# Kernel optimization log

Measured on AMD Instinct MI355X. Metric: run time of the kernel, lower is better.

## Reference

```python
import jax, jax.numpy as jnp
import numpy as np

N, D = 16384, 64      # samples, state dimension (input_size)
H1, H2 = 256, 256     # hidden widths


def setup_inputs() -> dict:
    key = jax.random.key(0)
    ks = jax.random.split(key, 7)
    S = jax.random.normal(ks[0], (N, D), jnp.float32)
    Sdot = jax.random.normal(ks[1], (N, D), jnp.float32)
    W1 = jax.random.normal(ks[2], (H1, D), jnp.float32) / np.float32(np.sqrt(D))
    b1 = jax.random.normal(ks[3], (H1,), jnp.float32) * 0.1
    W2 = jax.random.normal(ks[4], (H2, H1), jnp.float32) / np.float32(np.sqrt(H1))
    b2 = jax.random.normal(ks[5], (H2,), jnp.float32) * 0.1
    W3 = jax.random.normal(ks[6], (1, H2), jnp.float32) / np.float32(np.sqrt(H2))
    return {"S": S, "Sdot": Sdot, "W1": W1, "b1": b1, "W2": W2, "b2": b2, "W3": W3}


def _forward_tensors(S, layers, W_last):
    # Manual MLP forward with per-sample Jacobian propagation.
    # SQUARE activation: act(z) = z^2, act'(z) = 2z.
    # torch's diag_embed(act_der) @ J is fused as elementwise row-scaling.
    n, d = S.shape
    y = S
    J = jnp.broadcast_to(jnp.eye(d, dtype=S.dtype), (n, d, d))  # [N, d, d]
    for W, b in layers:
        z = y @ W.T + b                      # [N, h]
        J = jnp.einsum('hp,npd->nhd', W, J)  # W @ J per sample
        J = (2.0 * z)[:, :, None] * J        # diag(2z) @ J as row scaling
        y = z * z                            # SQUARE activation
    nn_out = (y @ W_last.T)[:, 0]            # [N]
    grad_nn = jnp.einsum('h,nhd->nd', W_last[0], J)  # [N, d]
    return nn_out, grad_nn


def reference(S, Sdot, W1, b1, W2, b2, W3):
    nn_out, grad_nn = _forward_tensors(S, [(W1, b1), (W2, b2)], W3)
    circle = jnp.sum(S * S, axis=1)          # [N]
    F = circle
    dF = 2.0 * S
    V = nn_out * F
    gradV = nn_out[:, None] * dF + grad_nn * F[:, None]  # product rule
    Vdot = jnp.sum(gradV * Sdot, axis=1)
    return (V, Vdot, circle)
```

## Files before the change

### kernel.cpp

```cpp
#include <hip/hip_runtime.h>

typedef __attribute__((ext_vector_type(8))) short bf16x8;
typedef __attribute__((ext_vector_type(4))) float f32x4;

constexpr int N  = 16384;
constexpr int D  = 64;
constexpr int H  = 256;
constexpr int SB = 32;
constexpr int PITCH = 272;
constexpr int PLANE = 32 * PITCH;
constexpr int STAGE = 8 * PITCH;

__device__ __forceinline__ ushort f2bf(float x) {
    uint u = __float_as_uint(x);
    u += 0x7fffu + ((u >> 16) & 1u);
    return (ushort)(u >> 16);
}
__device__ __forceinline__ float bf2f(ushort h) {
    return __uint_as_float(((uint)h) << 16);
}
__device__ __forceinline__ int swz(int g, int i) {
    return i ^ ((i >> 2) & 3) ^ ((g & 1) << 1);
}

__global__ void prep_weights(const float* __restrict__ W1, const float* __restrict__ W2,
                             ushort* __restrict__ ws) {
    const int t = blockIdx.x * 256 + threadIdx.x;
    if (t < 8192) {
        const int h1g = t >> 8;
        const int h2  = t & 255;
        const float* src = W2 + h2 * 256 + h1g * 8;
        bf16x8 hi;
        #pragma unroll
        for (int j = 0; j < 8; ++j) hi[j] = (short)f2bf(src[j]);
        *reinterpret_cast<bf16x8*>(ws + 32768 + (h1g * 256 + h2) * 8) = hi;
    } else if (t < 10240) {
        const int u  = t - 8192;
        const int dg = u >> 8;
        const int h1 = u & 255;
        const float* src = W1 + h1 * 64 + dg * 8;
        bf16x8 hi, lo;
        #pragma unroll
        for (int j = 0; j < 8; ++j) {
            const float x = src[j];
            const ushort xh = f2bf(x);
            hi[j] = (short)xh;
            lo[j] = (short)f2bf(x - bf2f(xh));
        }
        const int d1 = (dg * 256 + h1) * 8;
        *reinterpret_cast<bf16x8*>(ws + d1)         = hi;
        *reinterpret_cast<bf16x8*>(ws + 16384 + d1) = lo;
    }
}

__global__ __launch_bounds__(256, 2) void fused_mfma(
    const float* __restrict__ S,  const float* __restrict__ Sdot,
    const float* __restrict__ b1v, const float* __restrict__ b2v,
    const float* __restrict__ W3, const ushort* __restrict__ ws,
    float* __restrict__ out)
{
    __shared__ ushort U[4 * STAGE + 2 * PLANE];
    __shared__ float  red[2][4][32];
    __shared__ float  csd[32][2];

    ushort* const sH = U;
    ushort* const sL = U + STAGE;
    ushort* const dH = U + 2 * STAGE;
    ushort* const dL = U + 3 * STAGE;
    ushort* const yH = U + 4 * STAGE;
    ushort* const pH = U + 4 * STAGE + PLANE;

    const int t   = threadIdx.x;
    const int l   = t & 63;
    const int wid = t >> 6;
    const int lg  = l >> 4;
    const int lc  = l & 15;
    const int s0  = blockIdx.x * SB;

    int hh[4];
    #pragma unroll
    for (int tt = 0; tt < 4; ++tt) hh[tt] = (wid * 4 + tt) * 16 + lc;

    bf16x8 B1h[2][4], B1l[2][4];
    #pragma unroll
    for (int kc = 0; kc < 2; ++kc) {
        const int g = kc * 4 + lg;
        #pragma unroll
        for (int tt = 0; tt < 4; ++tt) {
            const int o = (g * 256 + hh[tt]) * 8;
            B1h[kc][tt] = *reinterpret_cast<const bf16x8*>(ws + o);
            B1l[kc][tt] = *reinterpret_cast<const bf16x8*>(ws + 16384 + o);
        }
    }
    bf16x8 nbh[4];
    #pragma unroll
    for (int tt = 0; tt < 4; ++tt)
        nbh[tt] = *reinterpret_cast<const bf16x8*>(ws + 32768 + (lg * 256 + hh[tt]) * 8);

    float bb1[4], bb2[4], w3v[4];
    #pragma unroll
    for (int tt = 0; tt < 4; ++tt) {
        bb1[tt] = b1v[hh[tt]]; bb2[tt] = b2v[hh[tt]]; w3v[tt] = W3[hh[tt]];
    }

    {
        const int i = t >> 3;
        const int g = t & 7;
        const float* sp = S    + (size_t)(s0 + i) * D + g * 8;
        const float* dp = Sdot + (size_t)(s0 + i) * D + g * 8;
        const float4 s_a = reinterpret_cast<const float4*>(sp)[0];
        const float4 s_b = reinterpret_cast<const float4*>(sp)[1];
        const float4 d_a = reinterpret_cast<const float4*>(dp)[0];
        const float4 d_b = reinterpret_cast<const float4*>(dp)[1];
        const float sv[8] = {s_a.x,s_a.y,s_a.z,s_a.w,s_b.x,s_b.y,s_b.z,s_b.w};
        const float dv[8] = {d_a.x,d_a.y,d_a.z,d_a.w,d_b.x,d_b.y,d_b.z,d_b.w};
        bf16x8 vsh, vsl, vdh, vdl;
        float c = 0.f, sd = 0.f;
        #pragma unroll
        for (int j = 0; j < 8; ++j) {
            c  += sv[j] * sv[j];
            sd += sv[j] * dv[j];
            const ushort hs = f2bf(sv[j]);
            vsh[j] = (short)hs; vsl[j] = (short)f2bf(sv[j] - bf2f(hs));
            const ushort hd = f2bf(dv[j]);
            vdh[j] = (short)hd; vdl[j] = (short)f2bf(dv[j] - bf2f(hd));
        }
        const int off = g * PITCH + swz(g, i) * 8;
        *reinterpret_cast<bf16x8*>(&sH[off]) = vsh;
        *reinterpret_cast<bf16x8*>(&sL[off]) = vsl;
        *reinterpret_cast<bf16x8*>(&dH[off]) = vdh;
        *reinterpret_cast<bf16x8*>(&dL[off]) = vdl;
        #pragma unroll
        for (int o = 1; o < 8; o <<= 1) { c += __shfl_xor(c, o); sd += __shfl_xor(sd, o); }
        if (g == 0) { csd[i][0] = c; csd[i][1] = sd; }
    }
    __syncthreads();

    f32x4 z1acc[2][4], u1acc[2][4];
    #pragma unroll
    for (int mt = 0; mt < 2; ++mt)
        #pragma unroll
        for (int tt = 0; tt < 4; ++tt) {
            z1acc[mt][tt] = (f32x4){0,0,0,0};
            u1acc[mt][tt] = (f32x4){0,0,0,0};
        }
    #pragma unroll
    for (int kc = 0; kc < 2; ++kc) {
        const int g = kc * 4 + lg;
        bf16x8 ash[2], asl[2], adh[2], adl[2];
        #pragma unroll
        for (int mt = 0; mt < 2; ++mt) {
            const int off = g * PITCH + swz(g, mt * 16 + lc) * 8;
            ash[mt] = *reinterpret_cast<const bf16x8*>(&sH[off]);
            asl[mt] = *reinterpret_cast<const bf16x8*>(&sL[off]);
            adh[mt] = *reinterpret_cast<const bf16x8*>(&dH[off]);
            adl[mt] = *reinterpret_cast<const bf16x8*>(&dL[off]);
        }
        __builtin_amdgcn_s_setprio(1);
        #pragma unroll
        for (int tt = 0; tt < 4; ++tt) {
            #pragma unroll
            for (int mt = 0; mt < 2; ++mt) {
                z1acc[mt][tt] = __builtin_amdgcn_mfma_f32_16x16x32_bf16(ash[mt], B1h[kc][tt], z1acc[mt][tt], 0,0,0);
                z1acc[mt][tt] = __builtin_amdgcn_mfma_f32_16x16x32_bf16(asl[mt], B1h[kc][tt], z1acc[mt][tt], 0,0,0);
                z1acc[mt][tt] = __builtin_amdgcn_mfma_f32_16x16x32_bf16(ash[mt], B1l[kc][tt], z1acc[mt][tt], 0,0,0);
                u1acc[mt][tt] = __builtin_amdgcn_mfma_f32_16x16x32_bf16(adh[mt], B1h[kc][tt], u1acc[mt][tt], 0,0,0);
                u1acc[mt][tt] = __builtin_amdgcn_mfma_f32_16x16x32_bf16(adl[mt], B1h[kc][tt], u1acc[mt][tt], 0,0,0);
                u1acc[mt][tt] = __builtin_amdgcn_mfma_f32_16x16x32_bf16(adh[mt], B1l[kc][tt], u1acc[mt][tt], 0,0,0);
            }
        }
        __builtin_amdgcn_s_setprio(0);
    }

    #pragma unroll
    for (int tt = 0; tt < 4; ++tt) {
        const int grp = hh[tt] >> 3;
        const int jb  = grp * PITCH + (hh[tt] & 7);
        #pragma unroll
        for (int mt = 0; mt < 2; ++mt) {
            #pragma unroll
            for (int r = 0; r < 4; ++r) {
                const float z  = z1acc[mt][tt][r] + bb1[tt];
                const float pv = 2.f * z * u1acc[mt][tt][r];
                const int ii = swz(grp, mt * 16 + lg * 4 + r);
                yH[jb + ii * 8] = f2bf(z * z);
                pH[jb + ii * 8] = f2bf(pv);
            }
        }
    }
    __syncthreads();

    f32x4 z2acc[2][4], qacc[2][4];
    #pragma unroll
    for (int mt = 0; mt < 2; ++mt)
        #pragma unroll
        for (int tt = 0; tt < 4; ++tt) {
            z2acc[mt][tt] = (f32x4){0,0,0,0};
            qacc[mt][tt]  = (f32x4){0,0,0,0};
        }
    #pragma unroll 2
    for (int kc = 0; kc < 8; ++kc) {
        const int g = kc * 4 + lg;
        bf16x8 bh[4];
        #pragma unroll
        for (int tt = 0; tt < 4; ++tt) bh[tt] = nbh[tt];
        if (kc < 7) {
            const int gn = (kc + 1) * 4 + lg;
            #pragma unroll
            for (int tt = 0; tt < 4; ++tt)
                nbh[tt] = *reinterpret_cast<const bf16x8*>(ws + 32768 + (gn * 256 + hh[tt]) * 8);
        }
        bf16x8 ayh[2], aph[2];
        #pragma unroll
        for (int mt = 0; mt < 2; ++mt) {
            const int off = g * PITCH + swz(g, mt * 16 + lc) * 8;
            ayh[mt] = *reinterpret_cast<const bf16x8*>(&yH[off]);
            aph[mt] = *reinterpret_cast<const bf16x8*>(&pH[off]);
        }
        __builtin_amdgcn_s_setprio(1);
        #pragma unroll
        for (int tt = 0; tt < 4; ++tt) {
            #pragma unroll
            for (int mt = 0; mt < 2; ++mt) {
                z2acc[mt][tt] = __builtin_amdgcn_mfma_f32_16x16x32_bf16(ayh[mt], bh[tt], z2acc[mt][tt], 0,0,0);
                qacc[mt][tt]  = __builtin_amdgcn_mfma_f32_16x16x32_bf16(aph[mt], bh[tt], qacc[mt][tt], 0,0,0);
            }
        }
        __builtin_amdgcn_s_setprio(0);
    }

    float nnp[2][4], gdp[2][4];
    #pragma unroll
    for (int mt = 0; mt < 2; ++mt)
        #pragma unroll
        for (int r = 0; r < 4; ++r) { nnp[mt][r] = 0.f; gdp[mt][r] = 0.f; }
    #pragma unroll
    for (int tt = 0; tt < 4; ++tt) {
        #pragma unroll
        for (int mt = 0; mt < 2; ++mt) {
            #pragma unroll
            for (int r = 0; r < 4; ++r) {
                const float z = z2acc[mt][tt][r] + bb2[tt];
                nnp[mt][r] += w3v[tt] * z * z;
                gdp[mt][r] += 2.f * w3v[tt] * z * qacc[mt][tt][r];
            }
        }
    }
    #pragma unroll
    for (int mt = 0; mt < 2; ++mt)
        #pragma unroll
        for (int r = 0; r < 4; ++r) {
            float a = nnp[mt][r], b = gdp[mt][r];
            #pragma unroll
            for (int o = 1; o < 16; o <<= 1) { a += __shfl_xor(a, o); b += __shfl_xor(b, o); }
            if (lc == 0) {
                red[0][wid][mt * 16 + lg * 4 + r] = a;
                red[1][wid][mt * 16 + lg * 4 + r] = b;
            }
        }
    __syncthreads();

    if (t < SB) {
        const int i = t;
        float nn = 0.f, gd = 0.f;
        #pragma unroll
        for (int w = 0; w < 4; ++w) { nn += red[0][w][i]; gd += red[1][w][i]; }
        const float c  = csd[i][0];
        const float sd = csd[i][1];
        const int n = s0 + i;
        out[n]         = nn * c;
        out[N + n]     = 2.f * nn * sd + c * gd;
        out[2 * N + n] = c;
    }
}

extern "C" void kernel_launch(void* const* d_in, const int* in_sizes, int n_in,
                              void* d_out, int out_size, void* d_ws, size_t ws_size,
                              hipStream_t stream) {
    const float* S    = (const float*)d_in[0];
    const float* Sdot = (const float*)d_in[1];
    const float* W1   = (const float*)d_in[2];
    const float* b1   = (const float*)d_in[3];
    const float* W2   = (const float*)d_in[4];
    const float* b2   = (const float*)d_in[5];
    const float* W3   = (const float*)d_in[6];
    float* out = (float*)d_out;
    ushort* ws = (ushort*)d_ws;

    prep_weights<<<40, 256, 0, stream>>>(W1, W2, ws);
    fused_mfma<<<N / SB, 256, 0, stream>>>(S, Sdot, b1, b2, W3, ws, out);
}
```

Before: 20.94 us.

## Split hidden dimension across eight waves per block instead of four

```diff
diff --git a/kernel.cpp b/kernel.cpp
--- a/kernel.cpp
+++ b/kernel.cpp
@@ -1,6 +1,7 @@
 #include <hip/hip_runtime.h>
 
 typedef __attribute__((ext_vector_type(8))) short bf16x8;
+typedef __attribute__((ext_vector_type(4))) short bf16x4;
 typedef __attribute__((ext_vector_type(4))) float f32x4;
 
 constexpr int N  = 16384;
@@ -53,14 +54,14 @@
     }
 }
 
-__global__ __launch_bounds__(256, 2) void fused_mfma(
+__global__ __launch_bounds__(512, 4) void fused_mfma(
     const float* __restrict__ S,  const float* __restrict__ Sdot,
     const float* __restrict__ b1v, const float* __restrict__ b2v,
     const float* __restrict__ W3, const ushort* __restrict__ ws,
     float* __restrict__ out)
 {
     __shared__ ushort U[4 * STAGE + 2 * PLANE];
-    __shared__ float  red[2][4][32];
+    __shared__ float  red[2][8][32];
     __shared__ float  csd[32][2];
 
     ushort* const sH = U;
@@ -77,47 +78,27 @@
     const int lc  = l & 15;
     const int s0  = blockIdx.x * SB;
 
-    int hh[4];
-    #pragma unroll
-    for (int tt = 0; tt < 4; ++tt) hh[tt] = (wid * 4 + tt) * 16 + lc;
-
-    bf16x8 B1h[2][4], B1l[2][4];
-    #pragma unroll
-    for (int kc = 0; kc < 2; ++kc) {
-        const int g = kc * 4 + lg;
-        #pragma unroll
-        for (int tt = 0; tt < 4; ++tt) {
-            const int o = (g * 256 + hh[tt]) * 8;
-            B1h[kc][tt] = *reinterpret_cast<const bf16x8*>(ws + o);
-            B1l[kc][tt] = *reinterpret_cast<const bf16x8*>(ws + 16384 + o);
-        }
-    }
-    bf16x8 nbh[4];
-    #pragma unroll
-    for (int tt = 0; tt < 4; ++tt)
-        nbh[tt] = *reinterpret_cast<const bf16x8*>(ws + 32768 + (lg * 256 + hh[tt]) * 8);
-
-    float bb1[4], bb2[4], w3v[4];
-    #pragma unroll
-    for (int tt = 0; tt < 4; ++tt) {
-        bb1[tt] = b1v[hh[tt]]; bb2[tt] = b2v[hh[tt]]; w3v[tt] = W3[hh[tt]];
-    }
+    const int hA = (wid * 2 + 0) * 16 + lc;
+    const int hB = (wid * 2 + 1) * 16 + lc;
+
+    const float bb1[2] = { b1v[hA], b1v[hB] };
+    const float bb2[2] = { b2v[hA], b2v[hB] };
+    const float w3v[2] = { W3[hA],  W3[hB]  };
 
     {
-        const int i = t >> 3;
-        const int g = t & 7;
-        const float* sp = S    + (size_t)(s0 + i) * D + g * 8;
-        const float* dp = Sdot + (size_t)(s0 + i) * D + g * 8;
-        const float4 s_a = reinterpret_cast<const float4*>(sp)[0];
-        const float4 s_b = reinterpret_cast<const float4*>(sp)[1];
-        const float4 d_a = reinterpret_cast<const float4*>(dp)[0];
-        const float4 d_b = reinterpret_cast<const float4*>(dp)[1];
-        const float sv[8] = {s_a.x,s_a.y,s_a.z,s_a.w,s_b.x,s_b.y,s_b.z,s_b.w};
-        const float dv[8] = {d_a.x,d_a.y,d_a.z,d_a.w,d_b.x,d_b.y,d_b.z,d_b.w};
-        bf16x8 vsh, vsl, vdh, vdl;
+        const int i    = t >> 4;
+        const int sub  = t & 15;
+        const int g    = sub >> 1;
+        const int half = sub & 1;
+        const size_t rb = (size_t)(s0 + i) * D + g * 8 + half * 4;
+        const float4 s4 = *reinterpret_cast<const float4*>(S    + rb);
+        const float4 d4 = *reinterpret_cast<const float4*>(Sdot + rb);
+        const float sv[4] = {s4.x, s4.y, s4.z, s4.w};
+        const float dv[4] = {d4.x, d4.y, d4.z, d4.w};
+        bf16x4 vsh, vsl, vdh, vdl;
         float c = 0.f, sd = 0.f;
         #pragma unroll
-        for (int j = 0; j < 8; ++j) {
+        for (int j = 0; j < 4; ++j) {
             c  += sv[j] * sv[j];
             sd += sv[j] * dv[j];
             const ushort hs = f2bf(sv[j]);
@@ -125,28 +106,37 @@
             const ushort hd = f2bf(dv[j]);
             vdh[j] = (short)hd; vdl[j] = (short)f2bf(dv[j] - bf2f(hd));
         }
-        const int off = g * PITCH + swz(g, i) * 8;
-        *reinterpret_cast<bf16x8*>(&sH[off]) = vsh;
-        *reinterpret_cast<bf16x8*>(&sL[off]) = vsl;
-        *reinterpret_cast<bf16x8*>(&dH[off]) = vdh;
-        *reinterpret_cast<bf16x8*>(&dL[off]) = vdl;
-        #pragma unroll
-        for (int o = 1; o < 8; o <<= 1) { c += __shfl_xor(c, o); sd += __shfl_xor(sd, o); }
-        if (g == 0) { csd[i][0] = c; csd[i][1] = sd; }
+        const int off = g * PITCH + swz(g, i) * 8 + half * 4;
+        *reinterpret_cast<bf16x4*>(&sH[off]) = vsh;
+        *reinterpret_cast<bf16x4*>(&sL[off]) = vsl;
+        *reinterpret_cast<bf16x4*>(&dH[off]) = vdh;
+        *reinterpret_cast<bf16x4*>(&dL[off]) = vdl;
+        #pragma unroll
+        for (int o = 1; o < 16; o <<= 1) { c += __shfl_xor(c, o); sd += __shfl_xor(sd, o); }
+        if (sub == 0) { csd[i][0] = c; csd[i][1] = sd; }
     }
     __syncthreads();
 
-    f32x4 z1acc[2][4], u1acc[2][4];
-    #pragma unroll
-    for (int mt = 0; mt < 2; ++mt)
-        #pragma unroll
-        for (int tt = 0; tt < 4; ++tt) {
+    f32x4 z1acc[2][2], u1acc[2][2];
+    #pragma unroll
+    for (int mt = 0; mt < 2; ++mt)
+        #pragma unroll
+        for (int tt = 0; tt < 2; ++tt) {
             z1acc[mt][tt] = (f32x4){0,0,0,0};
             u1acc[mt][tt] = (f32x4){0,0,0,0};
         }
     #pragma unroll
     for (int kc = 0; kc < 2; ++kc) {
         const int g = kc * 4 + lg;
+        bf16x8 bh[2], bl[2];
+        {
+            const int oA = (g * 256 + hA) * 8;
+            const int oB = (g * 256 + hB) * 8;
+            bh[0] = *reinterpret_cast<const bf16x8*>(ws + oA);
+            bh[1] = *reinterpret_cast<const bf16x8*>(ws + oB);
+            bl[0] = *reinterpret_cast<const bf16x8*>(ws + 16384 + oA);
+            bl[1] = *reinterpret_cast<const bf16x8*>(ws + 16384 + oB);
+        }
         bf16x8 ash[2], asl[2], adh[2], adl[2];
         #pragma unroll
         for (int mt = 0; mt < 2; ++mt) {
@@ -158,24 +148,29 @@
         }
         __builtin_amdgcn_s_setprio(1);
         #pragma unroll
-        for (int tt = 0; tt < 4; ++tt) {
+        for (int tt = 0; tt < 2; ++tt) {
             #pragma unroll
             for (int mt = 0; mt < 2; ++mt) {
-                z1acc[mt][tt] = __builtin_amdgcn_mfma_f32_16x16x32_bf16(ash[mt], B1h[kc][tt], z1acc[mt][tt], 0,0,0);
-                z1acc[mt][tt] = __builtin_amdgcn_mfma_f32_16x16x32_bf16(asl[mt], B1h[kc][tt], z1acc[mt][tt], 0,0,0);
-                z1acc[mt][tt] = __builtin_amdgcn_mfma_f32_16x16x32_bf16(ash[mt], B1l[kc][tt], z1acc[mt][tt], 0,0,0);
-                u1acc[mt][tt] = __builtin_amdgcn_mfma_f32_16x16x32_bf16(adh[mt], B1h[kc][tt], u1acc[mt][tt], 0,0,0);
-                u1acc[mt][tt] = __builtin_amdgcn_mfma_f32_16x16x32_bf16(adl[mt], B1h[kc][tt], u1acc[mt][tt], 0,0,0);
-                u1acc[mt][tt] = __builtin_amdgcn_mfma_f32_16x16x32_bf16(adh[mt], B1l[kc][tt], u1acc[mt][tt], 0,0,0);
+                z1acc[mt][tt] = __builtin_amdgcn_mfma_f32_16x16x32_bf16(ash[mt], bh[tt], z1acc[mt][tt], 0,0,0);
+                z1acc[mt][tt] = __builtin_amdgcn_mfma_f32_16x16x32_bf16(asl[mt], bh[tt], z1acc[mt][tt], 0,0,0);
+                z1acc[mt][tt] = __builtin_amdgcn_mfma_f32_16x16x32_bf16(ash[mt], bl[tt], z1acc[mt][tt], 0,0,0);
+                u1acc[mt][tt] = __builtin_amdgcn_mfma_f32_16x16x32_bf16(adh[mt], bh[tt], u1acc[mt][tt], 0,0,0);
+                u1acc[mt][tt] = __builtin_amdgcn_mfma_f32_16x16x32_bf16(adl[mt], bh[tt], u1acc[mt][tt], 0,0,0);
+                u1acc[mt][tt] = __builtin_amdgcn_mfma_f32_16x16x32_bf16(adh[mt], bl[tt], u1acc[mt][tt], 0,0,0);
             }
         }
         __builtin_amdgcn_s_setprio(0);
     }
 
-    #pragma unroll
-    for (int tt = 0; tt < 4; ++tt) {
-        const int grp = hh[tt] >> 3;
-        const int jb  = grp * PITCH + (hh[tt] & 7);
+    bf16x8 nbh[2];
+    nbh[0] = *reinterpret_cast<const bf16x8*>(ws + 32768 + (lg * 256 + hA) * 8);
+    nbh[1] = *reinterpret_cast<const bf16x8*>(ws + 32768 + (lg * 256 + hB) * 8);
+
+    #pragma unroll
+    for (int tt = 0; tt < 2; ++tt) {
+        const int h   = tt ? hB : hA;
+        const int grp = h >> 3;
+        const int jb  = grp * PITCH + (h & 7);
         #pragma unroll
         for (int mt = 0; mt < 2; ++mt) {
             #pragma unroll
@@ -190,25 +185,22 @@
     }
     __syncthreads();
 
-    f32x4 z2acc[2][4], qacc[2][4];
-    #pragma unroll
-    for (int mt = 0; mt < 2; ++mt)
-        #pragma unroll
-        for (int tt = 0; tt < 4; ++tt) {
+    f32x4 z2acc[2][2], qacc[2][2];
+    #pragma unroll
+    for (int mt = 0; mt < 2; ++mt)
+        #pragma unroll
+        for (int tt = 0; tt < 2; ++tt) {
             z2acc[mt][tt] = (f32x4){0,0,0,0};
             qacc[mt][tt]  = (f32x4){0,0,0,0};
         }
     #pragma unroll 2
     for (int kc = 0; kc < 8; ++kc) {
         const int g = kc * 4 + lg;
-        bf16x8 bh[4];
-        #pragma unroll
-        for (int tt = 0; tt < 4; ++tt) bh[tt] = nbh[tt];
+        const bf16x8 bh0 = nbh[0], bh1 = nbh[1];
         if (kc < 7) {
             const int gn = (kc + 1) * 4 + lg;
-            #pragma unroll
-            for (int tt = 0; tt < 4; ++tt)
-                nbh[tt] = *reinterpret_cast<const bf16x8*>(ws + 32768 + (gn * 256 + hh[tt]) * 8);
+            nbh[0] = *reinterpret_cast<const bf16x8*>(ws + 32768 + (gn * 256 + hA) * 8);
+            nbh[1] = *reinterpret_cast<const bf16x8*>(ws + 32768 + (gn * 256 + hB) * 8);
         }
         bf16x8 ayh[2], aph[2];
         #pragma unroll
@@ -219,12 +211,11 @@
         }
         __builtin_amdgcn_s_setprio(1);
         #pragma unroll
-        for (int tt = 0; tt < 4; ++tt) {
-            #pragma unroll
-            for (int mt = 0; mt < 2; ++mt) {
-                z2acc[mt][tt] = __builtin_amdgcn_mfma_f32_16x16x32_bf16(ayh[mt], bh[tt], z2acc[mt][tt], 0,0,0);
-                qacc[mt][tt]  = __builtin_amdgcn_mfma_f32_16x16x32_bf16(aph[mt], bh[tt], qacc[mt][tt], 0,0,0);
-            }
+        for (int mt = 0; mt < 2; ++mt) {
+            z2acc[mt][0] = __builtin_amdgcn_mfma_f32_16x16x32_bf16(ayh[mt], bh0, z2acc[mt][0], 0,0,0);
+            qacc[mt][0]  = __builtin_amdgcn_mfma_f32_16x16x32_bf16(aph[mt], bh0, qacc[mt][0], 0,0,0);
+            z2acc[mt][1] = __builtin_amdgcn_mfma_f32_16x16x32_bf16(ayh[mt], bh1, z2acc[mt][1], 0,0,0);
+            qacc[mt][1]  = __builtin_amdgcn_mfma_f32_16x16x32_bf16(aph[mt], bh1, qacc[mt][1], 0,0,0);
         }
         __builtin_amdgcn_s_setprio(0);
     }
@@ -235,7 +226,7 @@
         #pragma unroll
         for (int r = 0; r < 4; ++r) { nnp[mt][r] = 0.f; gdp[mt][r] = 0.f; }
     #pragma unroll
-    for (int tt = 0; tt < 4; ++tt) {
+    for (int tt = 0; tt < 2; ++tt) {
         #pragma unroll
         for (int mt = 0; mt < 2; ++mt) {
             #pragma unroll
@@ -264,7 +255,7 @@
         const int i = t;
         float nn = 0.f, gd = 0.f;
         #pragma unroll
-        for (int w = 0; w < 4; ++w) { nn += red[0][w][i]; gd += red[1][w][i]; }
+        for (int w = 0; w < 8; ++w) { nn += red[0][w][i]; gd += red[1][w][i]; }
         const float c  = csd[i][0];
         const float sd = csd[i][1];
         const int n = s0 + i;
@@ -288,5 +279,5 @@
     ushort* ws = (ushort*)d_ws;
 
     prep_weights<<<40, 256, 0, stream>>>(W1, W2, ws);
-    fused_mfma<<<N / SB, 256, 0, stream>>>(S, Sdot, b1, b2, W3, ws, out);
-}
+    fused_mfma<<<N / SB, 512, 0, stream>>>(S, Sdot, b1, b2, W3, ws, out);
+}
```

Result: slower. 21.90 us (+4.6%).
